# Performance work log

Measured on AMD Instinct MI355X. Metric: run time of the kernel, lower is better.

## Reference

```python
import jax, jax.numpy as jnp
import numpy as np

N = 8192
IN_F = 256
OUT_F = 64
ALPHA = 0.2
NEG_INF = -9e15


def setup_inputs() -> dict:
    key = jax.random.key(0)
    k1, k2, k3, k4 = jax.random.split(key, 4)
    h = jax.random.normal(k1, (N, IN_F), dtype=jnp.float32)
    W = jax.random.normal(k2, (IN_F, OUT_F), dtype=jnp.float32) * (1.414 / np.sqrt(IN_F))
    a = jax.random.normal(k3, (2 * OUT_F, 1), dtype=jnp.float32) * (1.414 / np.sqrt(2 * OUT_F))
    adj = jax.random.randint(k4, (N, N), 0, 2, dtype=jnp.int32)
    return {"h": h, "W": W, "a": a, "adj": adj}


def reference(h, W, a, adj):
    # Wh: [N, F]
    Wh = h @ W
    # Decompose concat-based attention: e_ij = LeakyReLU(Wh_i . a[:F] + Wh_j . a[F:])
    a1, a2 = a[:OUT_F], a[OUT_F:]
    src = Wh @ a1              # [N, 1] contribution of row i
    dst = Wh @ a2              # [N, 1] contribution of col j
    e = jax.nn.leaky_relu(src + dst.T, negative_slope=ALPHA)  # [N, N]
    e = jnp.where(adj > 0, e, NEG_INF)
    attention = jax.nn.softmax(e, axis=1)
    # dropout is identity in eval mode
    h_prime = attention @ Wh   # [N, F]
    return h_prime
```

## Files before the change

kernel.cpp:

```cpp
#include <hip/hip_runtime.h>

#define NROWS 8192
#define NSPLIT 8
#define JT (NROWS / NSPLIT)
#define L2E 1.4426950408889634f
#define MASKVAL -1.2984255368000352e16f

typedef __attribute__((ext_vector_type(4))) float f32x4;
typedef __attribute__((ext_vector_type(8))) __bf16 bf16x8;
typedef __attribute__((ext_vector_type(4))) unsigned int u32x4;

__device__ __forceinline__ unsigned short f2bf(float x) {
  unsigned u = __float_as_uint(x);
  u += 0x7fffu + ((u >> 16) & 1u);
  return (unsigned short)(u >> 16);
}

__global__ __launch_bounds__(256) void k_prep(
    const float* __restrict__ h, const float* __restrict__ W,
    const float* __restrict__ a, unsigned short* __restrict__ WhB,
    float* __restrict__ src, float* __restrict__ dst) {
  int i = blockIdx.x * 4 + (threadIdx.x >> 6);
  int lane = threadIdx.x & 63;
  const float* hrow = h + (size_t)i * 256;
  float s = 0.f;
#pragma unroll 4
  for (int k = 0; k < 256; k += 4) {
    float4 hv = *(const float4*)(hrow + k);
    s = fmaf(hv.x, W[(k + 0) * 64 + lane], s);
    s = fmaf(hv.y, W[(k + 1) * 64 + lane], s);
    s = fmaf(hv.z, W[(k + 2) * 64 + lane], s);
    s = fmaf(hv.w, W[(k + 3) * 64 + lane], s);
  }
  int nt = lane >> 4, c = lane & 15;
  int gi = (i >> 3) & 3, e = i & 7;
  int idx = ((((i >> 5) * 4 + nt) * 64) + c + 16 * gi) * 8 + e;
  WhB[idx] = f2bf(s);
  float v1 = s * a[lane];
  float v2 = s * a[64 + lane];
#pragma unroll
  for (int d = 32; d; d >>= 1) {
    v1 += __shfl_xor(v1, d);
    v2 += __shfl_xor(v2, d);
  }
  if (lane == 0) {
    src[i] = v1 * L2E;
    dst[i] = v2 * L2E;
  }
}

__global__ __launch_bounds__(256, 4) void k_attn(
    const int* __restrict__ adj, const unsigned short* __restrict__ WhB,
    const float* __restrict__ src, const float* __restrict__ dst,
    float* __restrict__ pm, float* __restrict__ pl, float* __restrict__ pacc) {
  int task = blockIdx.x * 4 + (threadIdx.x >> 6);
  int sp = task >> 9;
  int mt = task & 511;
  int lane = threadIdx.x & 63;
  int r = lane & 15;
  int g = lane >> 4;
  int row0 = mt * 16;
  float srcr = src[row0 + r];
  float m = -INFINITY;
  float lrow = 0.f;
  f32x4 acc[4] = {f32x4{0.f, 0.f, 0.f, 0.f}, f32x4{0.f, 0.f, 0.f, 0.f},
                  f32x4{0.f, 0.f, 0.f, 0.f}, f32x4{0.f, 0.f, 0.f, 0.f}};
  int jbase = sp * JT;
  const int* adjp = adj + (size_t)(row0 + r) * NROWS + jbase + 8 * g;
  const float* dstp = dst + jbase + 8 * g;
  const bf16x8* Bfr = (const bf16x8*)WhB;

  int4 ca0 = *(const int4*)(adjp + 0);
  int4 ca1 = *(const int4*)(adjp + 4);
  int4 ca2 = *(const int4*)(adjp + 32);
  int4 ca3 = *(const int4*)(adjp + 36);

  for (int jb = 0; jb < JT; jb += 64) {
    float4 d0 = *(const float4*)(dstp + jb);
    float4 d1 = *(const float4*)(dstp + jb + 4);
    float4 d2 = *(const float4*)(dstp + jb + 32);
    float4 d3 = *(const float4*)(dstp + jb + 36);

    int jc = (jbase + jb) >> 5;
    const bf16x8* bp = Bfr + (size_t)jc * 256 + lane;
    bf16x8 b0 = bp[0];
    bf16x8 b1 = bp[64];
    bf16x8 b2 = bp[128];
    bf16x8 b3 = bp[192];
    bf16x8 b4 = bp[256];
    bf16x8 b5 = bp[320];
    bf16x8 b6 = bp[384];
    bf16x8 b7 = bp[448];
    __builtin_amdgcn_sched_barrier(0);

    int off = (jb + 64 < JT) ? (jb + 64) : 0;
    int4 na0 = *(const int4*)(adjp + off);
    int4 na1 = *(const int4*)(adjp + off + 4);
    int4 na2 = *(const int4*)(adjp + off + 32);
    int4 na3 = *(const int4*)(adjp + off + 36);
    __builtin_amdgcn_sched_barrier(0);

    float ev[16];
#define EC(aa, dd)                        \
  ({                                      \
    float v_ = srcr + (dd);               \
    v_ = fmaxf(v_, 0.2f * v_);            \
    ((aa) > 0) ? v_ : MASKVAL;            \
  })
    ev[0] = EC(ca0.x, d0.x);  ev[1] = EC(ca0.y, d0.y);
    ev[2] = EC(ca0.z, d0.z);  ev[3] = EC(ca0.w, d0.w);
    ev[4] = EC(ca1.x, d1.x);  ev[5] = EC(ca1.y, d1.y);
    ev[6] = EC(ca1.z, d1.z);  ev[7] = EC(ca1.w, d1.w);
    ev[8] = EC(ca2.x, d2.x);  ev[9] = EC(ca2.y, d2.y);
    ev[10] = EC(ca2.z, d2.z); ev[11] = EC(ca2.w, d2.w);
    ev[12] = EC(ca3.x, d3.x); ev[13] = EC(ca3.y, d3.y);
    ev[14] = EC(ca3.z, d3.z); ev[15] = EC(ca3.w, d3.w);
#undef EC

    float cm = ev[0];
#pragma unroll
    for (int t = 1; t < 16; t++) cm = fmaxf(cm, ev[t]);
    cm = fmaxf(cm, __shfl_xor(cm, 16));
    cm = fmaxf(cm, __shfl_xor(cm, 32));
    float mnew = fmaxf(m, cm);

    float ps = 0.f;
    unsigned q[8];
#pragma unroll
    for (int t = 0; t < 16; t += 2) {
      float p0 = exp2f(ev[t] - mnew);
      float p1 = exp2f(ev[t + 1] - mnew);
      ps += p0 + p1;
      unsigned qq;
      asm("v_cvt_pk_bf16_f32 %0, %1, %2" : "=v"(qq) : "v"(p0), "v"(p1));
      q[t >> 1] = qq;
    }
    ps += __shfl_xor(ps, 16);
    ps += __shfl_xor(ps, 32);

    if (__any(mnew > m)) {
      float sc = exp2f(m - mnew);
      float s0 = __shfl(sc, 4 * g + 0);
      float s1 = __shfl(sc, 4 * g + 1);
      float s2 = __shfl(sc, 4 * g + 2);
      float s3 = __shfl(sc, 4 * g + 3);
#pragma unroll
      for (int nt = 0; nt < 4; nt++) {
        acc[nt][0] *= s0;
        acc[nt][1] *= s1;
        acc[nt][2] *= s2;
        acc[nt][3] *= s3;
      }
      lrow = lrow * sc + ps;
    } else {
      lrow += ps;
    }
    m = mnew;

    u32x4 qv0 = {q[0], q[1], q[2], q[3]};
    u32x4 qv1 = {q[4], q[5], q[6], q[7]};
    bf16x8 A0 = __builtin_bit_cast(bf16x8, qv0);
    bf16x8 A1 = __builtin_bit_cast(bf16x8, qv1);

    __builtin_amdgcn_s_setprio(1);
    acc[0] = __builtin_amdgcn_mfma_f32_16x16x32_bf16(A0, b0, acc[0], 0, 0, 0);
    acc[1] = __builtin_amdgcn_mfma_f32_16x16x32_bf16(A0, b1, acc[1], 0, 0, 0);
    acc[2] = __builtin_amdgcn_mfma_f32_16x16x32_bf16(A0, b2, acc[2], 0, 0, 0);
    acc[3] = __builtin_amdgcn_mfma_f32_16x16x32_bf16(A0, b3, acc[3], 0, 0, 0);
    acc[0] = __builtin_amdgcn_mfma_f32_16x16x32_bf16(A1, b4, acc[0], 0, 0, 0);
    acc[1] = __builtin_amdgcn_mfma_f32_16x16x32_bf16(A1, b5, acc[1], 0, 0, 0);
    acc[2] = __builtin_amdgcn_mfma_f32_16x16x32_bf16(A1, b6, acc[2], 0, 0, 0);
    acc[3] = __builtin_amdgcn_mfma_f32_16x16x32_bf16(A1, b7, acc[3], 0, 0, 0);
    __builtin_amdgcn_s_setprio(0);

    ca0 = na0; ca1 = na1; ca2 = na2; ca3 = na3;
  }

  if (lane < 16) {
    pm[sp * NROWS + row0 + lane] = m;
    pl[sp * NROWS + row0 + lane] = lrow;
  }
#pragma unroll
  for (int nt = 0; nt < 4; nt++)
#pragma unroll
    for (int q2 = 0; q2 < 4; q2++)
      pacc[((size_t)sp * NROWS + row0 + 4 * g + q2) * 64 + nt * 16 + r] = acc[nt][q2];
}

__global__ __launch_bounds__(256) void k_comb(
    const float* __restrict__ pm, const float* __restrict__ pl,
    const float* __restrict__ pacc, float* __restrict__ out) {
  int t = blockIdx.x * 256 + threadIdx.x;
  int row = t >> 6, f = t & 63;
  float mv[NSPLIT];
  float M = -INFINITY;
#pragma unroll
  for (int s2 = 0; s2 < NSPLIT; s2++) {
    mv[s2] = pm[s2 * NROWS + row];
    M = fmaxf(M, mv[s2]);
  }
  float L = 0.f, o = 0.f;
#pragma unroll
  for (int s2 = 0; s2 < NSPLIT; s2++) {
    float w = exp2f(mv[s2] - M);
    L += pl[s2 * NROWS + row] * w;
    o += pacc[((size_t)s2 * NROWS + row) * 64 + f] * w;
  }
  out[t] = o / L;
}

extern "C" void kernel_launch(void* const* d_in, const int* in_sizes, int n_in,
                              void* d_out, int out_size, void* d_ws, size_t ws_size,
                              hipStream_t stream) {
  const float* h = (const float*)d_in[0];
  const float* W = (const float*)d_in[1];
  const float* a = (const float*)d_in[2];
  const int* adj = (const int*)d_in[3];
  float* out = (float*)d_out;

  char* ws = (char*)d_ws;
  unsigned short* WhB = (unsigned short*)ws;
  float* src = (float*)(ws + (1 << 20));
  float* dst = (float*)(ws + (1 << 20) + 32768);
  float* pm = (float*)(ws + (1 << 20) + 65536);
  float* pl = (float*)(ws + (1 << 20) + 65536 + NSPLIT * NROWS * 4);
  float* pacc = (float*)(ws + (1 << 20) + 65536 + 2 * NSPLIT * NROWS * 4);

  hipLaunchKernelGGL(k_prep, dim3(NROWS / 4), dim3(256), 0, stream, h, W, a, WhB, src, dst);
  hipLaunchKernelGGL(k_attn, dim3(512 * NSPLIT / 4), dim3(256), 0, stream,
                     adj, WhB, src, dst, pm, pl, pacc);
  hipLaunchKernelGGL(k_comb, dim3(NROWS * 64 / 256), dim3(256), 0, stream, pm, pl, pacc, out);
}
```

Before: 123.3 us.

## Replace online softmax with a precomputed global row-max bound

Adds a small kernel that computes the global maximum of dst. Each row then uses LeakyReLU(src_i + max dst) as a fixed upper bound for the softmax exponent, which removes the per-tile running max, the rescaling of the accumulators and the cross-split max combine. The dst slice is staged in shared memory, and the j-loop is fully unrolled with double-buffered adjacency registers. In exchange it adds an extra launch, and underflow is possible if a row's true max is far below the bound, since masked entries become exact zeros.

```diff
diff --git a/kernel.cpp b/kernel.cpp
--- a/kernel.cpp
+++ b/kernel.cpp
@@ -3,8 +3,8 @@
 #define NROWS 8192
 #define NSPLIT 8
 #define JT (NROWS / NSPLIT)
+#define NITER (JT / 64)
 #define L2E 1.4426950408889634f
-#define MASKVAL -1.2984255368000352e16f
 
 typedef __attribute__((ext_vector_type(4))) float f32x4;
 typedef __attribute__((ext_vector_type(8))) __bf16 bf16x8;
@@ -49,10 +49,25 @@
   }
 }
 
+__global__ __launch_bounds__(256) void k_dmax(
+    const float* __restrict__ dst, float* __restrict__ dmax) {
+  __shared__ float red[4];
+  float v = -INFINITY;
+  for (int i = threadIdx.x; i < NROWS; i += 256) v = fmaxf(v, dst[i]);
+#pragma unroll
+  for (int d = 32; d; d >>= 1) v = fmaxf(v, __shfl_xor(v, d));
+  if ((threadIdx.x & 63) == 0) red[threadIdx.x >> 6] = v;
+  __syncthreads();
+  if (threadIdx.x == 0)
+    *dmax = fmaxf(fmaxf(red[0], red[1]), fmaxf(red[2], red[3]));
+}
+
 __global__ __launch_bounds__(256, 4) void k_attn(
     const int* __restrict__ adj, const unsigned short* __restrict__ WhB,
     const float* __restrict__ src, const float* __restrict__ dst,
-    float* __restrict__ pm, float* __restrict__ pl, float* __restrict__ pacc) {
+    const float* __restrict__ dmax,
+    float* __restrict__ pl, float* __restrict__ pacc) {
+  __shared__ float ldst[JT];
   int task = blockIdx.x * 4 + (threadIdx.x >> 6);
   int sp = task >> 9;
   int mt = task & 511;
@@ -60,26 +75,32 @@
   int r = lane & 15;
   int g = lane >> 4;
   int row0 = mt * 16;
+  int jbase = sp * JT;
+
+  for (int k = threadIdx.x; k < JT; k += 256) ldst[k] = dst[jbase + k];
+  __syncthreads();
+
   float srcr = src[row0 + r];
-  float m = -INFINITY;
+  float dmv = *dmax;
+  float vB = srcr + dmv;
+  float Mi = fmaxf(vB, 0.2f * vB);
+
   float lrow = 0.f;
   f32x4 acc[4] = {f32x4{0.f, 0.f, 0.f, 0.f}, f32x4{0.f, 0.f, 0.f, 0.f},
                   f32x4{0.f, 0.f, 0.f, 0.f}, f32x4{0.f, 0.f, 0.f, 0.f}};
-  int jbase = sp * JT;
   const int* adjp = adj + (size_t)(row0 + r) * NROWS + jbase + 8 * g;
-  const float* dstp = dst + jbase + 8 * g;
   const bf16x8* Bfr = (const bf16x8*)WhB;
 
-  int4 ca0 = *(const int4*)(adjp + 0);
-  int4 ca1 = *(const int4*)(adjp + 4);
-  int4 ca2 = *(const int4*)(adjp + 32);
-  int4 ca3 = *(const int4*)(adjp + 36);
-
-  for (int jb = 0; jb < JT; jb += 64) {
-    float4 d0 = *(const float4*)(dstp + jb);
-    float4 d1 = *(const float4*)(dstp + jb + 4);
-    float4 d2 = *(const float4*)(dstp + jb + 32);
-    float4 d3 = *(const float4*)(dstp + jb + 36);
+  int4 ab[2][4];
+  ab[0][0] = *(const int4*)(adjp + 0);
+  ab[0][1] = *(const int4*)(adjp + 4);
+  ab[0][2] = *(const int4*)(adjp + 32);
+  ab[0][3] = *(const int4*)(adjp + 36);
+
+#pragma unroll
+  for (int it = 0; it < NITER; ++it) {
+    const int jb = it * 64;
+    const int cur = it & 1, nxt = cur ^ 1;
 
     int jc = (jbase + jb) >> 5;
     const bf16x8* bp = Bfr + (size_t)jc * 256 + lane;
@@ -93,70 +114,46 @@
     bf16x8 b7 = bp[448];
     __builtin_amdgcn_sched_barrier(0);
 
-    int off = (jb + 64 < JT) ? (jb + 64) : 0;
-    int4 na0 = *(const int4*)(adjp + off);
-    int4 na1 = *(const int4*)(adjp + off + 4);
-    int4 na2 = *(const int4*)(adjp + off + 32);
-    int4 na3 = *(const int4*)(adjp + off + 36);
+    const int* ap = adjp + ((it < NITER - 1) ? jb + 64 : 0);
+    ab[nxt][0] = *(const int4*)(ap + 0);
+    ab[nxt][1] = *(const int4*)(ap + 4);
+    ab[nxt][2] = *(const int4*)(ap + 32);
+    ab[nxt][3] = *(const int4*)(ap + 36);
     __builtin_amdgcn_sched_barrier(0);
 
-    float ev[16];
-#define EC(aa, dd)                        \
-  ({                                      \
-    float v_ = srcr + (dd);               \
+    const float4* dl = (const float4*)(ldst + jb + 8 * g);
+    float4 d0 = dl[0];
+    float4 d1 = dl[1];
+    const float4* dl2 = (const float4*)(ldst + jb + 32 + 8 * g);
+    float4 d2 = dl2[0];
+    float4 d3 = dl2[1];
+
+    float p[16];
+#define PE(P, AA, DD)                     \
+  {                                       \
+    float v_ = srcr + (DD);               \
     v_ = fmaxf(v_, 0.2f * v_);            \
-    ((aa) > 0) ? v_ : MASKVAL;            \
-  })
-    ev[0] = EC(ca0.x, d0.x);  ev[1] = EC(ca0.y, d0.y);
-    ev[2] = EC(ca0.z, d0.z);  ev[3] = EC(ca0.w, d0.w);
-    ev[4] = EC(ca1.x, d1.x);  ev[5] = EC(ca1.y, d1.y);
-    ev[6] = EC(ca1.z, d1.z);  ev[7] = EC(ca1.w, d1.w);
-    ev[8] = EC(ca2.x, d2.x);  ev[9] = EC(ca2.y, d2.y);
-    ev[10] = EC(ca2.z, d2.z); ev[11] = EC(ca2.w, d2.w);
-    ev[12] = EC(ca3.x, d3.x); ev[13] = EC(ca3.y, d3.y);
-    ev[14] = EC(ca3.z, d3.z); ev[15] = EC(ca3.w, d3.w);
-#undef EC
-
-    float cm = ev[0];
-#pragma unroll
-    for (int t = 1; t < 16; t++) cm = fmaxf(cm, ev[t]);
-    cm = fmaxf(cm, __shfl_xor(cm, 16));
-    cm = fmaxf(cm, __shfl_xor(cm, 32));
-    float mnew = fmaxf(m, cm);
-
-    float ps = 0.f;
+    float e_ = exp2f(v_ - Mi);            \
+    (P) = ((AA) > 0) ? e_ : 0.f;          \
+  }
+    PE(p[0], ab[cur][0].x, d0.x) PE(p[1], ab[cur][0].y, d0.y)
+    PE(p[2], ab[cur][0].z, d0.z) PE(p[3], ab[cur][0].w, d0.w)
+    PE(p[4], ab[cur][1].x, d1.x) PE(p[5], ab[cur][1].y, d1.y)
+    PE(p[6], ab[cur][1].z, d1.z) PE(p[7], ab[cur][1].w, d1.w)
+    PE(p[8], ab[cur][2].x, d2.x) PE(p[9], ab[cur][2].y, d2.y)
+    PE(p[10], ab[cur][2].z, d2.z) PE(p[11], ab[cur][2].w, d2.w)
+    PE(p[12], ab[cur][3].x, d3.x) PE(p[13], ab[cur][3].y, d3.y)
+    PE(p[14], ab[cur][3].z, d3.z) PE(p[15], ab[cur][3].w, d3.w)
+#undef PE
+
     unsigned q[8];
 #pragma unroll
     for (int t = 0; t < 16; t += 2) {
-      float p0 = exp2f(ev[t] - mnew);
-      float p1 = exp2f(ev[t + 1] - mnew);
-      ps += p0 + p1;
+      lrow += p[t] + p[t + 1];
       unsigned qq;
-      asm("v_cvt_pk_bf16_f32 %0, %1, %2" : "=v"(qq) : "v"(p0), "v"(p1));
+      asm("v_cvt_pk_bf16_f32 %0, %1, %2" : "=v"(qq) : "v"(p[t]), "v"(p[t + 1]));
       q[t >> 1] = qq;
     }
-    ps += __shfl_xor(ps, 16);
-    ps += __shfl_xor(ps, 32);
-
-    if (__any(mnew > m)) {
-      float sc = exp2f(m - mnew);
-      float s0 = __shfl(sc, 4 * g + 0);
-      float s1 = __shfl(sc, 4 * g + 1);
-      float s2 = __shfl(sc, 4 * g + 2);
-      float s3 = __shfl(sc, 4 * g + 3);
-#pragma unroll
-      for (int nt = 0; nt < 4; nt++) {
-        acc[nt][0] *= s0;
-        acc[nt][1] *= s1;
-        acc[nt][2] *= s2;
-        acc[nt][3] *= s3;
-      }
-      lrow = lrow * sc + ps;
-    } else {
-      lrow += ps;
-    }
-    m = mnew;
-
     u32x4 qv0 = {q[0], q[1], q[2], q[3]};
     u32x4 qv1 = {q[4], q[5], q[6], q[7]};
     bf16x8 A0 = __builtin_bit_cast(bf16x8, qv0);
@@ -172,14 +169,11 @@
     acc[2] = __builtin_amdgcn_mfma_f32_16x16x32_bf16(A1, b6, acc[2], 0, 0, 0);
     acc[3] = __builtin_amdgcn_mfma_f32_16x16x32_bf16(A1, b7, acc[3], 0, 0, 0);
     __builtin_amdgcn_s_setprio(0);
-
-    ca0 = na0; ca1 = na1; ca2 = na2; ca3 = na3;
-  }
-
-  if (lane < 16) {
-    pm[sp * NROWS + row0 + lane] = m;
-    pl[sp * NROWS + row0 + lane] = lrow;
-  }
+  }
+
+  lrow += __shfl_xor(lrow, 16);
+  lrow += __shfl_xor(lrow, 32);
+  if (lane < 16) pl[sp * NROWS + row0 + lane] = lrow;
 #pragma unroll
   for (int nt = 0; nt < 4; nt++)
 #pragma unroll
@@ -188,23 +182,15 @@
 }
 
 __global__ __launch_bounds__(256) void k_comb(
-    const float* __restrict__ pm, const float* __restrict__ pl,
-    const float* __restrict__ pacc, float* __restrict__ out) {
+    const float* __restrict__ pl, const float* __restrict__ pacc,
+    float* __restrict__ out) {
   int t = blockIdx.x * 256 + threadIdx.x;
   int row = t >> 6, f = t & 63;
-  float mv[NSPLIT];
-  float M = -INFINITY;
+  float L = 0.f, o = 0.f;
 #pragma unroll
   for (int s2 = 0; s2 < NSPLIT; s2++) {
-    mv[s2] = pm[s2 * NROWS + row];
-    M = fmaxf(M, mv[s2]);
-  }
-  float L = 0.f, o = 0.f;
-#pragma unroll
-  for (int s2 = 0; s2 < NSPLIT; s2++) {
-    float w = exp2f(mv[s2] - M);
-    L += pl[s2 * NROWS + row] * w;
-    o += pacc[((size_t)s2 * NROWS + row) * 64 + f] * w;
+    L += pl[s2 * NROWS + row];
+    o += pacc[((size_t)s2 * NROWS + row) * 64 + f];
   }
   out[t] = o / L;
 }
@@ -220,14 +206,15 @@
 
   char* ws = (char*)d_ws;
   unsigned short* WhB = (unsigned short*)ws;
-  float* src = (float*)(ws + (1 << 20));
-  float* dst = (float*)(ws + (1 << 20) + 32768);
-  float* pm = (float*)(ws + (1 << 20) + 65536);
-  float* pl = (float*)(ws + (1 << 20) + 65536 + NSPLIT * NROWS * 4);
-  float* pacc = (float*)(ws + (1 << 20) + 65536 + 2 * NSPLIT * NROWS * 4);
+  float* src = (float*)(ws + 0x100000);
+  float* dst = (float*)(ws + 0x108000);
+  float* dmax = (float*)(ws + 0x110000);
+  float* pl = (float*)(ws + 0x110100);
+  float* pacc = (float*)(ws + 0x150100);
 
   hipLaunchKernelGGL(k_prep, dim3(NROWS / 4), dim3(256), 0, stream, h, W, a, WhB, src, dst);
+  hipLaunchKernelGGL(k_dmax, dim3(1), dim3(256), 0, stream, dst, dmax);
   hipLaunchKernelGGL(k_attn, dim3(512 * NSPLIT / 4), dim3(256), 0, stream,
-                     adj, WhB, src, dst, pm, pl, pacc);
-  hipLaunchKernelGGL(k_comb, dim3(NROWS * 64 / 256), dim3(256), 0, stream, pm, pl, pacc, out);
-}
+                     adj, WhB, src, dst, dmax, pl, pacc);
+  hipLaunchKernelGGL(k_comb, dim3(NROWS * 64 / 256), dim3(256), 0, stream, pl, pacc, out);
+}
```

Result: no change. 124.5 us (+1.0%).
